# Performance work log

Measured on AMD Instinct MI355X. Metric: run time of the kernel, lower is better.

The kernel has to match this reference:

```python
import jax, jax.numpy as jnp
import numpy as np

# Dims: N nodes, C channels (multiplicity), K = 9 input spherical comps (l=0,1,2),
# E elements, output irreps L in {0,1} with M_L = 2L+1, correlation nu = 3.
N, C, K, E = 1024, 128, 9, 10
M = {0: 1, 1: 3}
P = {1: 1, 2: 2, 3: 3}  # number of symmetric-contraction paths per correlation order


def setup_inputs() -> dict:
    key = jax.random.key(0)
    ks = iter(jax.random.split(key, 32))
    inp = {}
    inp["node_feats"] = jax.random.normal(next(ks), (N, C, K), jnp.float32)
    species = jax.random.randint(next(ks), (N,), 0, E)
    inp["node_attrs"] = jax.nn.one_hot(species, E, dtype=jnp.float32)
    inp["sc"] = jax.random.normal(next(ks), (N, C * (M[0] + M[1])), jnp.float32)
    # Generalized CG coefficient tensors U_t (fixed basis; random stand-ins with
    # the same shape/contraction structure as the real Clebsch-Gordan U matrices)
    # and learned element-dependent weights W_t, per output irrep L.
    for L in (0, 1):
        for t in (1, 2, 3):
            u = jax.random.normal(next(ks), (K,) * t + (M[L], P[t]), jnp.float32)
            inp[f"U{t}_{L}"] = u * (K ** (-0.5 * t))
            inp[f"W{t}_{L}"] = jax.random.normal(next(ks), (E, P[t], C), jnp.float32) / np.sqrt(P[t])
        inp[f"Wlin_{L}"] = jax.random.normal(next(ks), (C, C), jnp.float32)
    return inp


def _sym_contract(x, na, U1, U2, U3, W1, W2, W3):
    # x: [N,C,K] node features, na: [N,E] one-hot element attrs.
    # Per-node path weights: [N,P_t,C]
    w1 = jnp.einsum('ne,epc->npc', na, W1)
    w2 = jnp.einsum('ne,epc->npc', na, W2)
    w3 = jnp.einsum('ne,epc->npc', na, W3)
    # Horner-style recursion of MACE's Contraction (highest order first):
    out = jnp.einsum('ijkmp,npc,nck->ncmij', U3, w3, x)      # [N,C,M,K,K]
    ct = jnp.einsum('ijmp,npc->ncmij', U2, w2) + out
    out = jnp.einsum('ncmij,ncj->ncmi', ct, x)               # [N,C,M,K]
    ct = jnp.einsum('imp,npc->ncmi', U1, w1) + out
    out = jnp.einsum('ncmi,nci->ncm', ct, x)                 # [N,C,M]
    return out


def reference(node_feats, node_attrs, sc,
              U1_0, U2_0, U3_0, U1_1, U2_1, U3_1,
              W1_0, W2_0, W3_0, W1_1, W2_1, W3_1,
              Wlin_0, Wlin_1):
    y0 = _sym_contract(node_feats, node_attrs, U1_0, U2_0, U3_0, W1_0, W2_0, W3_0)  # [N,C,1]
    y1 = _sym_contract(node_feats, node_attrs, U1_1, U2_1, U3_1, W1_1, W2_1, W3_1)  # [N,C,3]
    inv = 1.0 / np.sqrt(node_feats.shape[1])  # e3nn Linear fan-in normalization
    z0 = jnp.einsum('ncm,cd->ndm', y0, Wlin_0) * inv
    z1 = jnp.einsum('ncm,cd->ndm', y1, Wlin_1) * inv
    n = node_feats.shape[0]
    out = jnp.concatenate([z0.reshape(n, -1), z1.reshape(n, -1)], axis=-1)  # [N, 512]
    return out + sc
```

## Files before the change

### kernel.cpp

```cpp
#include <hip/hip_runtime.h>


typedef __attribute__((ext_vector_type(8))) short short8;
typedef __attribute__((ext_vector_type(16))) float f32x16;

#define NSTEP 14
#define TBLB_DWORDS (NSTEP*64*4)
#define WL_OFF TBLB_DWORDS
#define TBLW_DWORDS (64*256)

static __device__ __forceinline__ short bf16b(float f) {
  __bf16 h = (__bf16)f;
  return __builtin_bit_cast(short, h);
}

struct Triples { unsigned char a[224], b[224], c3[224], ord[224]; };
constexpr Triples make_triples() {
  Triples T{};
  int s = 0;
  for (int i = 0; i < 9; ++i)
    for (int j = i; j < 9; ++j)
      for (int k = j; k < 9; ++k) { T.a[s]=(unsigned char)i; T.b[s]=(unsigned char)j; T.c3[s]=(unsigned char)k; T.ord[s]=3; ++s; }
  for (int i = 0; i < 9; ++i)
    for (int j = i; j < 9; ++j) { T.a[s]=(unsigned char)i; T.b[s]=(unsigned char)j; T.ord[s]=2; ++s; }
  for (int i = 0; i < 9; ++i) { T.a[s]=(unsigned char)i; T.ord[s]=1; ++s; }
  for (; s < 224; ++s) T.ord[s] = 0;
  return T;
}
static constexpr Triples TRI = make_triples();

template<int KI>
static __device__ __forceinline__ float monoT(const float* xr) {
  if constexpr (TRI.ord[KI] == 3) return xr[TRI.a[KI]] * xr[TRI.b[KI]] * xr[TRI.c3[KI]];
  else if constexpr (TRI.ord[KI] == 2) return xr[TRI.a[KI]] * xr[TRI.b[KI]];
  else if constexpr (TRI.ord[KI] == 1) return xr[TRI.a[KI]];
  else return 0.f;
}

template<int K0>
static __device__ __forceinline__ void mono8(const float* xr, float m[8]) {
  m[0]=monoT<K0+0>(xr); m[1]=monoT<K0+1>(xr); m[2]=monoT<K0+2>(xr); m[3]=monoT<K0+3>(xr);
  m[4]=monoT<K0+4>(xr); m[5]=monoT<K0+5>(xr); m[6]=monoT<K0+6>(xr); m[7]=monoT<K0+7>(xr);
}

template<int T>
static __device__ __forceinline__ void k_steps(const float* xr, const unsigned int* lds_b,
                                               int lane, int ks, f32x16& acc) {
  if constexpr (T < NSTEP) {
    float m[8];
    if (ks == 0) mono8<T*16>(xr, m);
    else         mono8<T*16 + 8>(xr, m);
    short8 mf;
    mf[0]=bf16b(m[0]); mf[1]=bf16b(m[1]); mf[2]=bf16b(m[2]); mf[3]=bf16b(m[3]);
    mf[4]=bf16b(m[4]); mf[5]=bf16b(m[5]); mf[6]=bf16b(m[6]); mf[7]=bf16b(m[7]);
    short8 cf = *(const short8*)&lds_b[(T*64 + lane)*4];
    acc = __builtin_amdgcn_mfma_f32_32x32x16_bf16(cf, mf, acc, 0, 0, 0);
    k_steps<T+1>(xr, lds_b, lane, ks, acc);
  }
}

static __device__ __forceinline__ float coefval(int k, int col,
    const float* U1_0, const float* U2_0, const float* U3_0,
    const float* U1_1, const float* U2_1, const float* U3_1) {
  if (k < 165) {
    if (col < 12 || col >= 24) return 0.f;
    int mp = (col - 12) / 3, p = (col - 12) % 3;
    int rem = k, I = 0;
    while (rem >= (9 - I) * (10 - I) / 2) { rem -= (9 - I) * (10 - I) / 2; ++I; }
    int J = I;
    while (rem >= 9 - J) { rem -= 9 - J; ++J; }
    int Kk = J + rem;
    int pm[6][3] = {{I,J,Kk},{I,Kk,J},{J,I,Kk},{J,Kk,I},{Kk,I,J},{Kk,J,I}};
    float acc = 0.f;
    for (int q = 0; q < 6; ++q) {
      bool dup = false;
      for (int r = 0; r < q; ++r)
        if (pm[r][0]==pm[q][0] && pm[r][1]==pm[q][1] && pm[r][2]==pm[q][2]) dup = true;
      if (dup) continue;
      int base = (pm[q][0]*9 + pm[q][1])*9 + pm[q][2];
      acc += (mp == 0) ? U3_0[base*3 + p] : U3_1[base*9 + (mp-1)*3 + p];
    }
    return acc;
  } else if (k < 210) {
    if (col < 4 || col >= 12) return 0.f;
    int mp = (col - 4) / 2, p = (col - 4) % 2;
    int rem = k - 165, I = 0;
    while (rem >= 9 - I) { rem -= 9 - I; ++I; }
    int J = I + rem;
    float acc = (mp == 0) ? U2_0[(I*9+J)*2 + p] : U2_1[((I*9+J)*3 + (mp-1))*2 + p];
    if (I != J) acc += (mp == 0) ? U2_0[(J*9+I)*2 + p] : U2_1[((J*9+I)*3 + (mp-1))*2 + p];
    return acc;
  } else if (k < 219) {
    int i = k - 210;
    if (col == 0) return U1_0[i];
    if (col < 4) return U1_1[i*3 + (col-1)];
    return 0.f;
  }
  return 0.f;
}

__global__ __launch_bounds__(64) void build_tables_kernel(
    const float* __restrict__ U1_0, const float* __restrict__ U2_0, const float* __restrict__ U3_0,
    const float* __restrict__ U1_1, const float* __restrict__ U2_1, const float* __restrict__ U3_1,
    const float* __restrict__ Wl0, const float* __restrict__ Wl1,
    unsigned int* __restrict__ tbl) {
  const int b = blockIdx.x, l = threadIdx.x;
  const int col = l & 31, ks = l >> 5;
  if (b < NSTEP) {
    const int ft = b;
    #pragma unroll
    for (int d = 0; d < 4; ++d) {
      int k = ft*16 + ks*8 + d*2;
      unsigned short lo = (unsigned short)bf16b(coefval(k,   col, U1_0,U2_0,U3_0,U1_1,U2_1,U3_1));
      unsigned short hi = (unsigned short)bf16b(coefval(k+1, col, U1_0,U2_0,U3_0,U1_1,U2_1,U3_1));
      tbl[(ft*64 + l)*4 + d] = ((unsigned int)hi << 16) | lo;
    }
  } else {
    const int u = b - NSTEP;
    const int g = u >> 5, u5 = u & 31, nt = u5 >> 3, st = u5 & 7;
    const float* W = g ? Wl1 : Wl0;
    #pragma unroll
    for (int d = 0; d < 4; ++d) {
      int k = st*16 + ks*8 + 2*d;
      unsigned short lo = (unsigned short)bf16b(W[(long)k*128     + nt*32 + col]);
      unsigned short hi = (unsigned short)bf16b(W[(long)(k+1)*128 + nt*32 + col]);
      tbl[WL_OFF + u*256 + l*4 + d] = ((unsigned int)hi << 16) | lo;
    }
  }
}

__global__ __launch_bounds__(512, 4) void epbb_mfma_kernel(
    const float* __restrict__ xg,
    const float* __restrict__ na,
    const float* __restrict__ sc,
    const float* __restrict__ W1_0, const float* __restrict__ W2_0, const float* __restrict__ W3_0,
    const float* __restrict__ W1_1, const float* __restrict__ W2_1, const float* __restrict__ W3_1,
    const unsigned int* __restrict__ tbl,
    float* __restrict__ out) {
  __shared__ __align__(16) unsigned int lds_b[TBLB_DWORDS];
  __shared__ __align__(16) short lds_yA[2][8][136];

  const int tid  = threadIdx.x;
  const int lane = tid & 63;
  const int w    = tid >> 6;
  const int ks   = lane >> 5;
  const int n0   = blockIdx.x * 2;

  for (int q = tid; q < TBLB_DWORDS; q += 512) lds_b[q] = tbl[q];

  const int nw = w >> 2;
  const int n  = n0 + nw;
  const int c0 = (w & 3) * 32;
  const int cl = c0 + (lane & 31);
  const float* xp = xg + ((long)(n*128 + cl))*9;
  float xr[9];
  #pragma unroll
  for (int q = 0; q < 9; ++q) xr[q] = xp[q];

  int e = 0;
  #pragma unroll
  for (int q = 0; q < 10; ++q) e = (na[(long)n*10 + q] > 0.5f) ? q : e;

  f32x16 acc;
  #pragma unroll
  for (int q = 0; q < 16; ++q) acc[q] = 0.f;

  __syncthreads();
  k_steps<0>(xr, lds_b, lane, ks, acc);

  const float w10  = W1_0[e*128 + cl];
  const float w20a = W2_0[(e*2+0)*128 + cl], w20b = W2_0[(e*2+1)*128 + cl];
  const float w30a = W3_0[(e*3+0)*128 + cl], w30b = W3_0[(e*3+1)*128 + cl], w30c = W3_0[(e*3+2)*128 + cl];
  const float w11  = W1_1[e*128 + cl];
  const float w21a = W2_1[(e*2+0)*128 + cl], w21b = W2_1[(e*2+1)*128 + cl];
  const float w31a = W3_1[(e*3+0)*128 + cl], w31b = W3_1[(e*3+1)*128 + cl], w31c = W3_1[(e*3+2)*128 + cl];

  float p0, p1, p2, p3;
  if (ks == 0) {
    p0 = w10*acc[0];
    p1 = w11*acc[1] + w31b*acc[8]  + w31c*acc[9];
    p2 = w11*acc[2] + w21a*acc[4]  + w21b*acc[5] + w31a*acc[10] + w31b*acc[11];
    p3 = w11*acc[3] + w21a*acc[6]  + w21b*acc[7];
  } else {
    p0 = w20a*acc[0] + w20b*acc[1] + w30a*acc[4] + w30b*acc[5] + w30c*acc[6];
    p1 = w21a*acc[2] + w21b*acc[3] + w31a*acc[7];
    p2 = w31c*acc[8];
    p3 = w31a*acc[9] + w31b*acc[10] + w31c*acc[11];
  }
  const float y0 = p0 + __shfl_xor(p0, 32, 64);
  const float y1 = p1 + __shfl_xor(p1, 32, 64);
  const float y2 = p2 + __shfl_xor(p2, 32, 64);
  const float y3 = p3 + __shfl_xor(p3, 32, 64);

  if (ks == 0) {
    lds_yA[0][nw][cl]     = bf16b(y0);
    lds_yA[1][nw][cl]     = bf16b(y1);
  } else {
    lds_yA[1][2 + nw][cl] = bf16b(y2);
    lds_yA[1][4 + nw][cl] = bf16b(y3);
  }
  __syncthreads();

  const int g  = w >> 2;
  const int nt = w & 3;
  f32x16 z;
  #pragma unroll
  for (int q = 0; q < 16; ++q) z[q] = 0.f;
  const unsigned int* bw = tbl + WL_OFF + ((g*4 + nt)*8)*256;
  #pragma unroll
  for (int st = 0; st < 8; ++st) {
    short8 af = *(const short8*)&lds_yA[g][lane & 7][st*16 + ks*8];
    short8 bf = *(const short8*)&bw[st*256 + lane*4];
    z = __builtin_amdgcn_mfma_f32_32x32x16_bf16(af, bf, z, 0, 0, 0);
  }
  const float inv = 0.088388347648318447f;
  const int d = nt*32 + (lane & 31);
  if (g == 0) {
    if (ks == 0) {
      #pragma unroll
      for (int r = 0; r < 2; ++r) {
        long o = (long)(n0 + r)*512 + d;
        out[o] = z[r]*inv + sc[o];
      }
    }
  } else {
    if (ks == 0) {
      #pragma unroll
      for (int r = 0; r < 4; ++r) {
        long o = (long)(n0 + (r & 1))*512 + 128 + 3*d + (r >> 1);
        out[o] = z[r]*inv + sc[o];
      }
    } else {
      #pragma unroll
      for (int r = 0; r < 2; ++r) {
        long o = (long)(n0 + r)*512 + 128 + 3*d + 2;
        out[o] = z[r]*inv + sc[o];
      }
    }
  }
}

extern "C" void kernel_launch(void* const* d_in, const int* in_sizes, int n_in,
                              void* d_out, int out_size, void* d_ws, size_t ws_size,
                              hipStream_t stream) {
  const float* xg   = (const float*)d_in[0];
  const float* na   = (const float*)d_in[1];
  const float* sc   = (const float*)d_in[2];
  const float* U1_0 = (const float*)d_in[3];
  const float* W1_0 = (const float*)d_in[4];
  const float* U2_0 = (const float*)d_in[5];
  const float* W2_0 = (const float*)d_in[6];
  const float* U3_0 = (const float*)d_in[7];
  const float* W3_0 = (const float*)d_in[8];
  const float* Wl0  = (const float*)d_in[9];
  const float* U1_1 = (const float*)d_in[10];
  const float* W1_1 = (const float*)d_in[11];
  const float* U2_1 = (const float*)d_in[12];
  const float* W2_1 = (const float*)d_in[13];
  const float* U3_1 = (const float*)d_in[14];
  const float* W3_1 = (const float*)d_in[15];
  const float* Wl1  = (const float*)d_in[16];

  unsigned int* tbl = (unsigned int*)d_ws;
  const int N = in_sizes[0] / (128 * 9);

  hipLaunchKernelGGL(build_tables_kernel, dim3(NSTEP + 64), dim3(64), 0, stream,
                     U1_0, U2_0, U3_0, U1_1, U2_1, U3_1, Wl0, Wl1, tbl);
  hipLaunchKernelGGL(epbb_mfma_kernel, dim3(N/2), dim3(512), 0, stream,
                     xg, na, sc, W1_0, W2_0, W3_0, W1_1, W2_1, W3_1, tbl,
                     (float*)d_out);
}
```

Before: 23.55 us.

## Read MFMA coefficient fragments from global memory instead of staging in LDS

The main kernel no longer copies the 14-step coefficient table into shared memory behind a barrier. Each wave now loads its B fragments straight from global memory (L2/L1-resident), and the per-element weight loads are hoisted ahead of the MFMA chain so their latency overlaps. The table-build kernel also swaps its runtime index decoding for constexpr lookup tables. This removes the per-block LDS fill and __syncthreads and cuts LDS use, which may raise occupancy, but it puts global-load latency on the MFMA critical path.

```diff
diff --git a/kernel.cpp b/kernel.cpp
--- a/kernel.cpp
+++ b/kernel.cpp
@@ -28,6 +28,37 @@
   return T;
 }
 static constexpr Triples TRI = make_triples();
+
+struct DecTab {
+  unsigned short b3[165][6]; unsigned char c3[165];
+  unsigned short b2[45][2];  unsigned char c2[45];
+};
+constexpr DecTab make_dectab() {
+  DecTab D{};
+  int s = 0;
+  for (int i = 0; i < 9; ++i)
+    for (int j = i; j < 9; ++j)
+      for (int k = j; k < 9; ++k) {
+        int pm[6][3] = {{i,j,k},{i,k,j},{j,i,k},{j,k,i},{k,i,j},{k,j,i}};
+        int cnt = 0;
+        for (int q = 0; q < 6; ++q) {
+          bool dup = false;
+          for (int r = 0; r < q; ++r)
+            if (pm[r][0]==pm[q][0] && pm[r][1]==pm[q][1] && pm[r][2]==pm[q][2]) dup = true;
+          if (!dup) { D.b3[s][cnt] = (unsigned short)((pm[q][0]*9 + pm[q][1])*9 + pm[q][2]); ++cnt; }
+        }
+        D.c3[s] = (unsigned char)cnt; ++s;
+      }
+  s = 0;
+  for (int i = 0; i < 9; ++i)
+    for (int j = i; j < 9; ++j) {
+      D.b2[s][0] = (unsigned short)(i*9 + j);
+      D.b2[s][1] = (unsigned short)(j*9 + i);
+      D.c2[s] = (unsigned char)((i == j) ? 1 : 2); ++s;
+    }
+  return D;
+}
+static constexpr DecTab DT = make_dectab();
 
 template<int KI>
 static __device__ __forceinline__ float monoT(const float* xr) {
@@ -44,7 +75,7 @@
 }
 
 template<int T>
-static __device__ __forceinline__ void k_steps(const float* xr, const unsigned int* lds_b,
+static __device__ __forceinline__ void k_steps(const float* xr, const unsigned int* __restrict__ tbl,
                                                int lane, int ks, f32x16& acc) {
   if constexpr (T < NSTEP) {
     float m[8];
@@ -53,9 +84,9 @@
     short8 mf;
     mf[0]=bf16b(m[0]); mf[1]=bf16b(m[1]); mf[2]=bf16b(m[2]); mf[3]=bf16b(m[3]);
     mf[4]=bf16b(m[4]); mf[5]=bf16b(m[5]); mf[6]=bf16b(m[6]); mf[7]=bf16b(m[7]);
-    short8 cf = *(const short8*)&lds_b[(T*64 + lane)*4];
+    short8 cf = *(const short8*)&tbl[(T*64 + lane)*4];
     acc = __builtin_amdgcn_mfma_f32_32x32x16_bf16(cf, mf, acc, 0, 0, 0);
-    k_steps<T+1>(xr, lds_b, lane, ks, acc);
+    k_steps<T+1>(xr, tbl, lane, ks, acc);
   }
 }
 
@@ -65,30 +96,23 @@
   if (k < 165) {
     if (col < 12 || col >= 24) return 0.f;
     int mp = (col - 12) / 3, p = (col - 12) % 3;
-    int rem = k, I = 0;
-    while (rem >= (9 - I) * (10 - I) / 2) { rem -= (9 - I) * (10 - I) / 2; ++I; }
-    int J = I;
-    while (rem >= 9 - J) { rem -= 9 - J; ++J; }
-    int Kk = J + rem;
-    int pm[6][3] = {{I,J,Kk},{I,Kk,J},{J,I,Kk},{J,Kk,I},{Kk,I,J},{Kk,J,I}};
     float acc = 0.f;
-    for (int q = 0; q < 6; ++q) {
-      bool dup = false;
-      for (int r = 0; r < q; ++r)
-        if (pm[r][0]==pm[q][0] && pm[r][1]==pm[q][1] && pm[r][2]==pm[q][2]) dup = true;
-      if (dup) continue;
-      int base = (pm[q][0]*9 + pm[q][1])*9 + pm[q][2];
+    int cnt = DT.c3[k];
+    for (int q = 0; q < cnt; ++q) {
+      int base = DT.b3[k][q];
       acc += (mp == 0) ? U3_0[base*3 + p] : U3_1[base*9 + (mp-1)*3 + p];
     }
     return acc;
   } else if (k < 210) {
     if (col < 4 || col >= 12) return 0.f;
     int mp = (col - 4) / 2, p = (col - 4) % 2;
-    int rem = k - 165, I = 0;
-    while (rem >= 9 - I) { rem -= 9 - I; ++I; }
-    int J = I + rem;
-    float acc = (mp == 0) ? U2_0[(I*9+J)*2 + p] : U2_1[((I*9+J)*3 + (mp-1))*2 + p];
-    if (I != J) acc += (mp == 0) ? U2_0[(J*9+I)*2 + p] : U2_1[((J*9+I)*3 + (mp-1))*2 + p];
+    int s2 = k - 165;
+    float acc = 0.f;
+    int cnt = DT.c2[s2];
+    for (int q = 0; q < cnt; ++q) {
+      int base = DT.b2[s2][q];
+      acc += (mp == 0) ? U2_0[base*2 + p] : U2_1[(base*3 + (mp-1))*2 + p];
+    }
     return acc;
   } else if (k < 219) {
     int i = k - 210;
@@ -137,7 +161,6 @@
     const float* __restrict__ W1_1, const float* __restrict__ W2_1, const float* __restrict__ W3_1,
     const unsigned int* __restrict__ tbl,
     float* __restrict__ out) {
-  __shared__ __align__(16) unsigned int lds_b[TBLB_DWORDS];
   __shared__ __align__(16) short lds_yA[2][8][136];
 
   const int tid  = threadIdx.x;
@@ -145,8 +168,6 @@
   const int w    = tid >> 6;
   const int ks   = lane >> 5;
   const int n0   = blockIdx.x * 2;
-
-  for (int q = tid; q < TBLB_DWORDS; q += 512) lds_b[q] = tbl[q];
 
   const int nw = w >> 2;
   const int n  = n0 + nw;
@@ -161,19 +182,18 @@
   #pragma unroll
   for (int q = 0; q < 10; ++q) e = (na[(long)n*10 + q] > 0.5f) ? q : e;
 
-  f32x16 acc;
-  #pragma unroll
-  for (int q = 0; q < 16; ++q) acc[q] = 0.f;
-
-  __syncthreads();
-  k_steps<0>(xr, lds_b, lane, ks, acc);
-
   const float w10  = W1_0[e*128 + cl];
   const float w20a = W2_0[(e*2+0)*128 + cl], w20b = W2_0[(e*2+1)*128 + cl];
   const float w30a = W3_0[(e*3+0)*128 + cl], w30b = W3_0[(e*3+1)*128 + cl], w30c = W3_0[(e*3+2)*128 + cl];
   const float w11  = W1_1[e*128 + cl];
   const float w21a = W2_1[(e*2+0)*128 + cl], w21b = W2_1[(e*2+1)*128 + cl];
   const float w31a = W3_1[(e*3+0)*128 + cl], w31b = W3_1[(e*3+1)*128 + cl], w31c = W3_1[(e*3+2)*128 + cl];
+
+  f32x16 acc;
+  #pragma unroll
+  for (int q = 0; q < 16; ++q) acc[q] = 0.f;
+
+  k_steps<0>(xr, tbl, lane, ks, acc);
 
   float p0, p1, p2, p3;
   if (ks == 0) {
```

Result: slower. 25.64 us (+8.8%).
